# Optimization experiments

Measured on AMD Instinct MI355X. Metric: run time of the kernel, lower is better.

## Reference

```python
import math
import jax, jax.numpy as jnp
import numpy as np

B, S, D, H = 2, 2048, 1024, 16
DK = D // H


def setup_inputs() -> dict:
    key = jax.random.key(0)
    ks = jax.random.split(key, 12)
    scale = 1.0 / math.sqrt(D)
    inp = {
        "q": jax.random.normal(ks[0], (B, S, D), jnp.float32),
        "k": jax.random.normal(ks[1], (B, S, D), jnp.float32),
        "v": jax.random.normal(ks[2], (B, S, D), jnp.float32),
        # causal mask, broadcast over batch and heads (mask==0 -> -inf)
        "mask": jnp.tril(jnp.ones((S, S), jnp.int32))[None, None, :, :],
        "Wq": jax.random.normal(ks[3], (D, D), jnp.float32) * scale,
        "bq": jnp.zeros((D,), jnp.float32),
        "Wk": jax.random.normal(ks[4], (D, D), jnp.float32) * scale,
        "bk": jnp.zeros((D,), jnp.float32),
        "Wv": jax.random.normal(ks[5], (D, D), jnp.float32) * scale,
        "bv": jnp.zeros((D,), jnp.float32),
        "Wo": jax.random.normal(ks[6], (D, D), jnp.float32) * scale,
        "bo": jnp.zeros((D,), jnp.float32),
    }
    return inp


def reference(q, k, v, mask, Wq, bq, Wk, bk, Wv, bv, Wo, bo):
    def proj(x, W, b):
        # [B,S,D] -> [B,H,S,DK]
        return (x @ W + b).reshape(B, -1, H, DK).transpose(0, 2, 1, 3)

    Q = proj(q, Wq, bq)
    K = proj(k, Wk, bk)
    V = proj(v, Wv, bv)
    scores = jnp.einsum("bhqd,bhkd->bhqk", Q, K) / math.sqrt(DK)  # [B,H,S,S]
    scores = jnp.where(mask == 0, -jnp.inf, scores)
    attn = jax.nn.softmax(scores, axis=-1)  # dropout p=0.0 -> identity
    ctx = jnp.einsum("bhqk,bhkd->bhqd", attn, V)
    ctx = ctx.transpose(0, 2, 1, 3).reshape(B, -1, D)  # [B,S,D]
    return ctx @ Wo + bo
```

## Files before the change

### kernel.cpp

```cpp
#include <hip/hip_runtime.h>
#include <stdint.h>

#define BB 2
#define SS 2048
#define DD 1024
#define HH 16
#define DK 64

#define QSCALE 0.1803368801111204f
#define NEGS -1.0e30f

typedef short s16x8 __attribute__((ext_vector_type(8)));
typedef float f32x4 __attribute__((ext_vector_type(4)));
typedef unsigned short u16x4 __attribute__((ext_vector_type(4)));
typedef unsigned int u32x4 __attribute__((ext_vector_type(4)));

static __device__ __forceinline__ unsigned short f2bf(float f) {
  unsigned int u = __builtin_bit_cast(unsigned int, f);
  u = (u + 0x7fffu + ((u >> 16) & 1u)) >> 16;
  return (unsigned short)u;
}

static __device__ __forceinline__ float bf2f(unsigned short s) {
  unsigned int u = ((unsigned int)s) << 16;
  return __builtin_bit_cast(float, u);
}

static __device__ __forceinline__ unsigned int cvtpk(float lo, float hi) {
  unsigned int r;
  asm("v_cvt_pk_bf16_f32 %0, %1, %2" : "=v"(r) : "v"(lo), "v"(hi));
  return r;
}

static __device__ __forceinline__ f32x4 mfma16(s16x8 a, s16x8 b, f32x4 c) {
  return __builtin_amdgcn_mfma_f32_16x16x32_bf16(a, b, c, 0, 0, 0);
}

static __device__ __forceinline__ void gload_lds16(const void* g, void* l) {
  __builtin_amdgcn_global_load_lds(
      (const __attribute__((address_space(1))) unsigned int*)g,
      (__attribute__((address_space(3))) unsigned int*)l, 16, 0, 0);
}

__global__ __launch_bounds__(256) void cvt3_kernel(const float* __restrict__ q,
                                                   const float* __restrict__ k,
                                                   const float* __restrict__ v,
                                                   unsigned short* __restrict__ qb,
                                                   unsigned short* __restrict__ kb,
                                                   unsigned short* __restrict__ vb) {
  int sel = blockIdx.y;
  const float* in = (sel == 0) ? q : ((sel == 1) ? k : v);
  unsigned short* out = (sel == 0) ? qb : ((sel == 1) ? kb : vb);
  int i = blockIdx.x * 256 + threadIdx.x;
  f32x4 vv = ((const f32x4*)in)[i];
  u16x4 o;
  o.x = f2bf(vv.x); o.y = f2bf(vv.y); o.z = f2bf(vv.z); o.w = f2bf(vv.w);
  ((u16x4*)out)[i] = o;
}

__global__ __launch_bounds__(256) void transpose_w4_kernel(const float* __restrict__ Wq,
                                                           const float* __restrict__ Wk,
                                                           const float* __restrict__ Wv,
                                                           const float* __restrict__ Wo,
                                                           unsigned short* __restrict__ WTbase) {
  __shared__ float t[32][33];
  int z = blockIdx.z;
  const float* W = (z == 0) ? Wq : ((z == 1) ? Wk : ((z == 2) ? Wv : Wo));
  float scale = (z == 0) ? QSCALE : 1.0f;
  unsigned short* WT = WTbase + (size_t)z * DD * DD;
  int n0 = blockIdx.x * 32, k0 = blockIdx.y * 32;
  int tx = threadIdx.x, ty = threadIdx.y;
  for (int i = 0; i < 4; ++i)
    t[ty + 8 * i][tx] = W[(size_t)(k0 + ty + 8 * i) * DD + n0 + tx];
  __syncthreads();
  for (int i = 0; i < 4; ++i)
    WT[(size_t)(n0 + ty + 8 * i) * DD + k0 + tx] = f2bf(t[tx][ty + 8 * i] * scale);
}

__global__ __launch_bounds__(256) void transpose_v_kernel(const unsigned short* __restrict__ V,
                                                          unsigned short* __restrict__ VT) {
  __shared__ unsigned short t[32][33];
  int s0 = blockIdx.x * 32, d0 = blockIdx.y * 32, bh = blockIdx.z;
  int tx = threadIdx.x, ty = threadIdx.y;
  const unsigned short* Vb = V + (size_t)bh * SS * DK;
  unsigned short* Tb = VT + (size_t)bh * DK * SS;
  for (int i = 0; i < 4; ++i)
    t[ty + 8 * i][tx] = Vb[(size_t)(s0 + ty + 8 * i) * DK + d0 + tx];
  __syncthreads();
  for (int i = 0; i < 4; ++i)
    Tb[(size_t)(d0 + ty + 8 * i) * SS + s0 + tx] = t[tx][ty + 8 * i];
}

__global__ __launch_bounds__(256) void gemm_qkv_kernel(
    const unsigned short* __restrict__ qb, const unsigned short* __restrict__ kb,
    const unsigned short* __restrict__ vb, const unsigned short* __restrict__ WTbase,
    const float* __restrict__ bq, const float* __restrict__ bk,
    const float* __restrict__ bv, unsigned short* __restrict__ Qh,
    unsigned short* __restrict__ Kh, unsigned short* __restrict__ Vh) {
  const int K = DD;
  __shared__ __align__(16) unsigned short Alds[128 * 32];
  __shared__ __align__(16) unsigned short Blds[128 * 32];
  int tid = threadIdx.x;
  int lane = tid & 63, wave = tid >> 6;
  int g = lane >> 4, r16 = lane & 15;
  int seg = blockIdx.y >> 5;
  int m0 = (blockIdx.y & 31) * 128, n0 = blockIdx.x * 128;
  int wm = (wave >> 1) * 64, wn = (wave & 1) * 64;

  const unsigned short* A = (seg == 0) ? qb : ((seg == 1) ? kb : vb);
  const unsigned short* BT = WTbase + (size_t)seg * DD * DD;
  const float* bias = (seg == 0) ? bq : ((seg == 1) ? bk : bv);
  unsigned short* outh = (seg == 0) ? Qh : ((seg == 1) ? Kh : Vh);
  float bsc = (seg == 0) ? QSCALE : 1.0f;

  f32x4 acc[4][4] = {};

  int c0 = tid, c1 = tid + 256;
  int arow0 = c0 >> 2, arow1 = c1 >> 2;
  int as0 = (c0 & 3) ^ ((arow0 >> 1) & 3);
  int as1 = (c1 & 3) ^ ((arow1 >> 1) & 3);

  for (int k0 = 0; k0 < K; k0 += 32) {
    __syncthreads();
    gload_lds16((const char*)(A + (size_t)(m0 + arow0) * K + k0) + as0 * 16,
                (char*)Alds + wave * 1024);
    gload_lds16((const char*)(A + (size_t)(m0 + arow1) * K + k0) + as1 * 16,
                (char*)Alds + wave * 1024 + 4096);
    gload_lds16((const char*)(BT + (size_t)(n0 + arow0) * K + k0) + as0 * 16,
                (char*)Blds + wave * 1024);
    gload_lds16((const char*)(BT + (size_t)(n0 + arow1) * K + k0) + as1 * 16,
                (char*)Blds + wave * 1024 + 4096);
    __syncthreads();

    s16x8 af[4], bfr[4];
#pragma unroll
    for (int mt = 0; mt < 4; ++mt) {
      int row = wm + mt * 16 + r16;
      int ch = g ^ ((row >> 1) & 3);
      af[mt] = *(const s16x8*)((const char*)Alds + row * 64 + ch * 16);
    }
#pragma unroll
    for (int nt = 0; nt < 4; ++nt) {
      int row = wn + nt * 16 + r16;
      int ch = g ^ ((row >> 1) & 3);
      bfr[nt] = *(const s16x8*)((const char*)Blds + row * 64 + ch * 16);
    }
#pragma unroll
    for (int mt = 0; mt < 4; ++mt)
#pragma unroll
      for (int nt = 0; nt < 4; ++nt)
        acc[mt][nt] = mfma16(af[mt], bfr[nt], acc[mt][nt]);
  }

#pragma unroll
  for (int nt = 0; nt < 4; ++nt) {
    int col = n0 + wn + nt * 16 + r16;
    int h = col >> 6, dk = col & (DK - 1);
    float bvv = bias[col] * bsc;
#pragma unroll
    for (int mt = 0; mt < 4; ++mt) {
#pragma unroll
      for (int rr = 0; rr < 4; ++rr) {
        int rowg = m0 + wm + mt * 16 + g * 4 + rr;
        int bb = rowg >> 11, s = rowg & (SS - 1);
        float val = acc[mt][nt][rr] + bvv;
        outh[(((size_t)bb * HH + h) * SS + s) * DK + dk] = f2bf(val);
      }
    }
  }
}

__global__ __launch_bounds__(256) void gemm_out_kernel(const unsigned short* __restrict__ A,
                                                       const unsigned short* __restrict__ BT,
                                                       const float* __restrict__ bias,
                                                       float* __restrict__ out) {
  const int K = DD;
  __shared__ __align__(16) unsigned short Alds[128 * 32];
  __shared__ __align__(16) unsigned short Blds[64 * 32];
  int tid = threadIdx.x;
  int lane = tid & 63, wave = tid >> 6;
  int g = lane >> 4, r16 = lane & 15;
  int m0 = blockIdx.y * 128, n0 = blockIdx.x * 64;
  int wm = (wave >> 1) * 64, wn = (wave & 1) * 32;

  f32x4 acc[4][2] = {};

  int c0 = tid, c1 = tid + 256;
  int arow0 = c0 >> 2, arow1 = c1 >> 2;
  int as0 = (c0 & 3) ^ ((arow0 >> 1) & 3);
  int as1 = (c1 & 3) ^ ((arow1 >> 1) & 3);

  for (int k0 = 0; k0 < K; k0 += 32) {
    __syncthreads();
    gload_lds16((const char*)(A + (size_t)(m0 + arow0) * K + k0) + as0 * 16,
                (char*)Alds + wave * 1024);
    gload_lds16((const char*)(A + (size_t)(m0 + arow1) * K + k0) + as1 * 16,
                (char*)Alds + wave * 1024 + 4096);
    gload_lds16((const char*)(BT + (size_t)(n0 + arow0) * K + k0) + as0 * 16,
                (char*)Blds + wave * 1024);
    __syncthreads();

    s16x8 af[4], bfr[2];
#pragma unroll
    for (int mt = 0; mt < 4; ++mt) {
      int row = wm + mt * 16 + r16;
      int ch = g ^ ((row >> 1) & 3);
      af[mt] = *(const s16x8*)((const char*)Alds + row * 64 + ch * 16);
    }
#pragma unroll
    for (int nt = 0; nt < 2; ++nt) {
      int row = wn + nt * 16 + r16;
      int ch = g ^ ((row >> 1) & 3);
      bfr[nt] = *(const s16x8*)((const char*)Blds + row * 64 + ch * 16);
    }
#pragma unroll
    for (int mt = 0; mt < 4; ++mt)
#pragma unroll
      for (int nt = 0; nt < 2; ++nt)
        acc[mt][nt] = mfma16(af[mt], bfr[nt], acc[mt][nt]);
  }

#pragma unroll
  for (int nt = 0; nt < 2; ++nt) {
    int col = n0 + wn + nt * 16 + r16;
    float bvv = bias[col];
#pragma unroll
    for (int mt = 0; mt < 4; ++mt) {
#pragma unroll
      for (int rr = 0; rr < 4; ++rr) {
        int rowg = m0 + wm + mt * 16 + g * 4 + rr;
        out[(size_t)rowg * DD + col] = acc[mt][nt][rr] + bvv;
      }
    }
  }
}

__global__ __launch_bounds__(256) void attn_kernel(const unsigned short* __restrict__ Qh,
                                                   const unsigned short* __restrict__ Kh,
                                                   const unsigned short* __restrict__ VhT,
                                                   unsigned short* __restrict__ ctx,
                                                   unsigned short* __restrict__ Opart,
                                                   float2* __restrict__ mlpart) {
  __shared__ __align__(16) unsigned short Klds[2][64 * 64];
  __shared__ __align__(16) unsigned short Vlds[2][64 * 64];

  int tid = threadIdx.x;
  int lane = tid & 63, wave = tid >> 6;
  int g = lane >> 4, r16 = lane & 15;
  int bid = blockIdx.x;
  int x = bid >> 3;
  int pid = x & 15;
  int hf = (x >> 4) & 1;
  int bh = ((x >> 5) << 3) | (bid & 7);

  int tilesA = hf ? 0 : pid + 1;
  int NT = hf ? 16 : 17;
  int q0A = pid * 64, q0B = (31 - pid) * 64;
  int kvoffB = hf ? (16 - pid) : 0;

  const unsigned short* Qb = Qh + (size_t)bh * SS * DK;
  const char* Kb = (const char*)(Kh + (size_t)bh * SS * DK);
  const char* Vb = (const char*)(VhT + (size_t)bh * DK * SS);

  int a_ = r16 >> 2, b_ = r16 & 3;
  int rbase = 8 * a_ + b_;
  int sk = b_ + 4 * (a_ & 1);

  int c0 = tid, c1 = tid + 256;
  int row0 = c0 >> 3, row1 = c1 >> 3;
  int skst0 = ((row0 & 3) | (((row0 >> 3) & 1) << 2));
  int skst1 = ((row1 & 3) | (((row1 >> 3) & 1) << 2));
  int kc0 = (c0 & 7) ^ skst0, kc1 = (c1 & 7) ^ skst1;
  int vc0 = (c0 & 7) ^ (row0 & 7), vc1 = (c1 & 7) ^ (row1 & 7);

#define KV_OF(t) ((hf ? (kvoffB + (t)) : (((t) < tilesA) ? (t) : ((t) - tilesA))) * 64)
#define STAGE_KV(buf, kv0)                                                   \
  do {                                                                       \
    gload_lds16(Kb + ((size_t)((kv0) + row0) * 128) + kc0 * 16,              \
                (char*)Klds[buf] + wave * 1024);                             \
    gload_lds16(Kb + ((size_t)((kv0) + row1) * 128) + kc1 * 16,              \
                (char*)Klds[buf] + wave * 1024 + 4096);                      \
    gload_lds16(Vb + ((size_t)row0 * SS + (kv0)) * 2 + vc0 * 16,             \
                (char*)Vlds[buf] + wave * 1024);                             \
    gload_lds16(Vb + ((size_t)row1 * SS + (kv0)) * 2 + vc1 * 16,             \
                (char*)Vlds[buf] + wave * 1024 + 4096);                      \
  } while (0)

  int b = bh >> 4, h = bh & (HH - 1);

  int qw0 = (hf ? q0B : q0A) + wave * 16;
  s16x8 aq[2];
#pragma unroll
  for (int kc = 0; kc < 2; ++kc)
    aq[kc] = *(const s16x8*)(Qb + (size_t)(qw0 + r16) * DK + kc * 32 + g * 8);

  STAGE_KV(0, KV_OF(0));

  f32x4 accd[4] = {};
  float mrow = -INFINITY, lrow = 0.0f;

  for (int t = 0; t < NT; ++t) {
    if (hf == 0 && t == tilesA) {
      float inv = 1.0f / lrow;
      int srow = qw0 + r16;
#pragma unroll
      for (int dsub = 0; dsub < 4; ++dsub) {
        int d0 = dsub * 16 + 4 * g;
        u16x4 o;
#pragma unroll
        for (int rr = 0; rr < 4; ++rr) o[rr] = f2bf(accd[dsub][rr] * inv);
        *(u16x4*)&ctx[(((size_t)b * SS + srow) * HH + h) * DK + d0] = o;
      }
      qw0 = q0B + wave * 16;
#pragma unroll
      for (int kc = 0; kc < 2; ++kc)
        aq[kc] = *(const s16x8*)(Qb + (size_t)(qw0 + r16) * DK + kc * 32 + g * 8);
#pragma unroll
      for (int dsub = 0; dsub < 4; ++dsub) accd[dsub] = (f32x4){0.f, 0.f, 0.f, 0.f};
      mrow = -INFINITY;
      lrow = 0.0f;
    }

    int kv0 = KV_OF(t);

    __syncthreads();
    if (t + 1 < NT) STAGE_KV((t + 1) & 1, KV_OF(t + 1));

    const char* Kc = (const char*)Klds[t & 1];
    const char* Vc = (const char*)Vlds[t & 1];

    f32x4 sf[4] = {};
    __builtin_amdgcn_s_setprio(1);
#pragma unroll
    for (int kc = 0; kc < 2; ++kc) {
      s16x8 bk[4];
#pragma unroll
      for (int nt = 0; nt < 4; ++nt) {
        int row = rbase + 4 * (nt & 1) + 32 * (nt >> 1);
        int ch = (kc * 4 + g) ^ sk;
        bk[nt] = *(const s16x8*)(Kc + row * 128 + ch * 16);
      }
#pragma unroll
      for (int nt = 0; nt < 4; ++nt)
        sf[nt] = mfma16(bk[nt], aq[kc], sf[nt]);
    }
    __builtin_amdgcn_s_setprio(0);

    s16x8 av[2][4];
#pragma unroll
    for (int c = 0; c < 2; ++c)
#pragma unroll
      for (int dsub = 0; dsub < 4; ++dsub) {
        int row = dsub * 16 + r16;
        int ch = (c * 4 + g) ^ (row & 7);
        av[c][dsub] = *(const s16x8*)(Vc + row * 128 + ch * 16);
      }

    if (kv0 + 63 > qw0) {
      int thr = qw0 + r16 - kv0 - 8 * g;
#pragma unroll
      for (int nt = 0; nt < 4; ++nt) {
        int koff = 4 * (nt & 1) + 32 * (nt >> 1);
#pragma unroll
        for (int rr = 0; rr < 4; ++rr)
          if (koff + rr > thr) sf[nt][rr] = NEGS;
      }
    }

    float tmax = NEGS;
#pragma unroll
    for (int nt = 0; nt < 4; ++nt)
#pragma unroll
      for (int rr = 0; rr < 4; ++rr) tmax = fmaxf(tmax, sf[nt][rr]);
    tmax = fmaxf(tmax, __shfl_xor(tmax, 16));
    tmax = fmaxf(tmax, __shfl_xor(tmax, 32));

    if (!__all(tmax <= mrow)) {
      float mn = fmaxf(mrow, tmax);
      float fc = __builtin_amdgcn_exp2f(mrow - mn);
      lrow *= fc;
      mrow = mn;
#pragma unroll
      for (int dsub = 0; dsub < 4; ++dsub)
#pragma unroll
        for (int rr = 0; rr < 4; ++rr) accd[dsub][rr] *= fc;
    }

    float pf[4][4];
    float su = 0.0f;
#pragma unroll
    for (int nt = 0; nt < 4; ++nt)
#pragma unroll
      for (int rr = 0; rr < 4; ++rr) {
        float p = __builtin_amdgcn_exp2f(sf[nt][rr] - mrow);
        pf[nt][rr] = p;
        su += p;
      }
    su += __shfl_xor(su, 16);
    su += __shfl_xor(su, 32);
    lrow += su;

    unsigned int pk[2][4];
#pragma unroll
    for (int c = 0; c < 2; ++c) {
      pk[c][0] = cvtpk(pf[2 * c][0], pf[2 * c][1]);
      pk[c][1] = cvtpk(pf[2 * c][2], pf[2 * c][3]);
      pk[c][2] = cvtpk(pf[2 * c + 1][0], pf[2 * c + 1][1]);
      pk[c][3] = cvtpk(pf[2 * c + 1][2], pf[2 * c + 1][3]);
    }

    __builtin_amdgcn_s_setprio(1);
#pragma unroll
    for (int c = 0; c < 2; ++c) {
      s16x8 pb = __builtin_bit_cast(s16x8, *(u32x4*)pk[c]);
#pragma unroll
      for (int dsub = 0; dsub < 4; ++dsub)
        accd[dsub] = mfma16(av[c][dsub], pb, accd[dsub]);
    }
    __builtin_amdgcn_s_setprio(0);
  }

  size_t prow = ((size_t)bh * 16 + pid) * 64 + wave * 16 + r16;
  float inv = 1.0f / lrow;
  unsigned short* Op = Opart + ((size_t)hf * 32768 + prow) * 64;
#pragma unroll
  for (int dsub = 0; dsub < 4; ++dsub) {
    int d0 = dsub * 16 + 4 * g;
    u16x4 o;
#pragma unroll
    for (int rr = 0; rr < 4; ++rr) o[rr] = f2bf(accd[dsub][rr] * inv);
    *(u16x4*)&Op[d0] = o;
  }
  if (g == 0) mlpart[(size_t)hf * 32768 + prow] = make_float2(mrow, lrow);
#undef STAGE_KV
#undef KV_OF
}

__global__ __launch_bounds__(256) void combine_kernel(const unsigned short* __restrict__ Opart,
                                                      const float2* __restrict__ mlpart,
                                                      unsigned short* __restrict__ ctx) {
  int idx = blockIdx.x * 256 + threadIdx.x;
  int row = idx >> 4;
  int d0 = (idx & 15) * 4;
  float2 ml0 = mlpart[row];
  float2 ml1 = mlpart[32768 + row];
  float m = fmaxf(ml0.x, ml1.x);
  float w0 = __builtin_amdgcn_exp2f(ml0.x - m) * ml0.y;
  float w1 = __builtin_amdgcn_exp2f(ml1.x - m) * ml1.y;
  float inv = 1.0f / (w0 + w1);
  w0 *= inv;
  w1 *= inv;
  u16x4 a = *(const u16x4*)(Opart + (size_t)row * 64 + d0);
  u16x4 bb4 = *(const u16x4*)(Opart + ((size_t)32768 + row) * 64 + d0);
  u16x4 o;
#pragma unroll
  for (int j = 0; j < 4; ++j) o[j] = f2bf(bf2f(a[j]) * w0 + bf2f(bb4[j]) * w1);
  int p = row >> 6, rin = row & 63;
  int bh = p >> 4, pid = p & 15;
  int srow = (31 - pid) * 64 + rin;
  int b = bh >> 4, h = bh & (HH - 1);
  *(u16x4*)&ctx[(((size_t)b * SS + srow) * HH + h) * DK + d0] = o;
}

extern "C" void kernel_launch(void* const* d_in, const int* in_sizes, int n_in,
                              void* d_out, int out_size, void* d_ws, size_t ws_size,
                              hipStream_t stream) {
  const float* q = (const float*)d_in[0];
  const float* k = (const float*)d_in[1];
  const float* v = (const float*)d_in[2];
  const float* Wq = (const float*)d_in[4];
  const float* bq = (const float*)d_in[5];
  const float* Wk = (const float*)d_in[6];
  const float* bk = (const float*)d_in[7];
  const float* Wv = (const float*)d_in[8];
  const float* bv = (const float*)d_in[9];
  const float* Wo = (const float*)d_in[10];
  const float* bo = (const float*)d_in[11];

  char* ws = (char*)d_ws;
  const size_t MB = 1ull << 20;
  unsigned short* qb = (unsigned short*)(ws + 0 * MB);
  unsigned short* kb = (unsigned short*)(ws + 8 * MB);
  unsigned short* vb = (unsigned short*)(ws + 16 * MB);
  unsigned short* WTbase = (unsigned short*)(ws + 24 * MB);
  unsigned short* WoT = (unsigned short*)(ws + 30 * MB);
  unsigned short* Qh = (unsigned short*)(ws + 32 * MB);
  unsigned short* Kh = (unsigned short*)(ws + 40 * MB);
  unsigned short* Vh = (unsigned short*)(ws + 48 * MB);
  unsigned short* VhT = (unsigned short*)(ws + 16 * MB);
  unsigned short* ctx = (unsigned short*)(ws + 0 * MB);
  unsigned short* Opart = (unsigned short*)(ws + 8 * MB);
  float2* mlpart = (float2*)(ws + 24 * MB);

  const int n4 = BB * SS * DD / 4;

  cvt3_kernel<<<dim3(n4 / 256, 3), 256, 0, stream>>>(q, k, v, qb, kb, vb);

  dim3 tb(32, 8);
  transpose_w4_kernel<<<dim3(32, 32, 4), tb, 0, stream>>>(Wq, Wk, Wv, Wo, WTbase);

  gemm_qkv_kernel<<<dim3(8, 96), 256, 0, stream>>>(qb, kb, vb, WTbase,
                                                   bq, bk, bv, Qh, Kh, Vh);

  transpose_v_kernel<<<dim3(SS / 32, DK / 32, BB * HH), tb, 0, stream>>>(Vh, VhT);

  attn_kernel<<<1024, 256, 0, stream>>>(Qh, Kh, VhT, ctx, Opart, mlpart);

  combine_kernel<<<2048, 256, 0, stream>>>(Opart, mlpart, ctx);

  gemm_out_kernel<<<dim3(16, 32), 256, 0, stream>>>(ctx, WoT, bo, (float*)d_out);
}
```

Before: 132.9 us.

## Fuse V transpose into QKV GEMM epilogue and double attention query tile per wave

The QKV GEMM now writes V directly in transposed [bh, dk, s] layout with vectorized stores, which removes the separate transpose_v kernel launch and its extra pass over memory. The attention kernel processes 128 query rows per block (32 per wave, as two 16-row MFMA tiles) instead of 64. Each K/V tile staged in LDS is therefore reused for twice as many queries, and the grid halves to 512 blocks. The causal pairing and the combine indexing are adjusted to match. The cost is higher register pressure and fewer blocks to fill the GPU.

New measurement: 140.5 us. +5.7%, slower.

```diff
diff --git a/kernel.cpp b/kernel.cpp
--- a/kernel.cpp
+++ b/kernel.cpp
@@ -77,26 +77,12 @@
     WT[(size_t)(n0 + ty + 8 * i) * DD + k0 + tx] = f2bf(t[tx][ty + 8 * i] * scale);
 }
 
-__global__ __launch_bounds__(256) void transpose_v_kernel(const unsigned short* __restrict__ V,
-                                                          unsigned short* __restrict__ VT) {
-  __shared__ unsigned short t[32][33];
-  int s0 = blockIdx.x * 32, d0 = blockIdx.y * 32, bh = blockIdx.z;
-  int tx = threadIdx.x, ty = threadIdx.y;
-  const unsigned short* Vb = V + (size_t)bh * SS * DK;
-  unsigned short* Tb = VT + (size_t)bh * DK * SS;
-  for (int i = 0; i < 4; ++i)
-    t[ty + 8 * i][tx] = Vb[(size_t)(s0 + ty + 8 * i) * DK + d0 + tx];
-  __syncthreads();
-  for (int i = 0; i < 4; ++i)
-    Tb[(size_t)(d0 + ty + 8 * i) * SS + s0 + tx] = t[tx][ty + 8 * i];
-}
-
 __global__ __launch_bounds__(256) void gemm_qkv_kernel(
     const unsigned short* __restrict__ qb, const unsigned short* __restrict__ kb,
     const unsigned short* __restrict__ vb, const unsigned short* __restrict__ WTbase,
     const float* __restrict__ bq, const float* __restrict__ bk,
     const float* __restrict__ bv, unsigned short* __restrict__ Qh,
-    unsigned short* __restrict__ Kh, unsigned short* __restrict__ Vh) {
+    unsigned short* __restrict__ Kh, unsigned short* __restrict__ VhT) {
   const int K = DD;
   __shared__ __align__(16) unsigned short Alds[128 * 32];
   __shared__ __align__(16) unsigned short Blds[128 * 32];
@@ -110,7 +96,6 @@
   const unsigned short* A = (seg == 0) ? qb : ((seg == 1) ? kb : vb);
   const unsigned short* BT = WTbase + (size_t)seg * DD * DD;
   const float* bias = (seg == 0) ? bq : ((seg == 1) ? bk : bv);
-  unsigned short* outh = (seg == 0) ? Qh : ((seg == 1) ? Kh : Vh);
   float bsc = (seg == 0) ? QSCALE : 1.0f;
 
   f32x4 acc[4][4] = {};
@@ -152,6 +137,7 @@
         acc[mt][nt] = mfma16(af[mt], bfr[nt], acc[mt][nt]);
   }
 
+  unsigned short* outh = (seg == 0) ? Qh : Kh;
 #pragma unroll
   for (int nt = 0; nt < 4; ++nt) {
     int col = n0 + wn + nt * 16 + r16;
@@ -159,12 +145,19 @@
     float bvv = bias[col] * bsc;
 #pragma unroll
     for (int mt = 0; mt < 4; ++mt) {
-#pragma unroll
-      for (int rr = 0; rr < 4; ++rr) {
-        int rowg = m0 + wm + mt * 16 + g * 4 + rr;
-        int bb = rowg >> 11, s = rowg & (SS - 1);
-        float val = acc[mt][nt][rr] + bvv;
-        outh[(((size_t)bb * HH + h) * SS + s) * DK + dk] = f2bf(val);
+      int row0g = m0 + wm + mt * 16 + g * 4;
+      int bb = row0g >> 11, s0 = row0g & (SS - 1);
+      if (seg == 2) {
+        u16x4 o;
+#pragma unroll
+        for (int rr = 0; rr < 4; ++rr) o[rr] = f2bf(acc[mt][nt][rr] + bvv);
+        *(u16x4*)&VhT[((size_t)(bb * HH + h) * DK + dk) * SS + s0] = o;
+      } else {
+#pragma unroll
+        for (int rr = 0; rr < 4; ++rr) {
+          outh[(((size_t)bb * HH + h) * SS + s0 + rr) * DK + dk] =
+              f2bf(acc[mt][nt][rr] + bvv);
+        }
       }
     }
   }
@@ -249,14 +242,14 @@
   int g = lane >> 4, r16 = lane & 15;
   int bid = blockIdx.x;
   int x = bid >> 3;
-  int pid = x & 15;
-  int hf = (x >> 4) & 1;
-  int bh = ((x >> 5) << 3) | (bid & 7);
-
-  int tilesA = hf ? 0 : pid + 1;
-  int NT = hf ? 16 : 17;
-  int q0A = pid * 64, q0B = (31 - pid) * 64;
-  int kvoffB = hf ? (16 - pid) : 0;
+  int pid = x & 7;
+  int hf = (x >> 3) & 1;
+  int bh = ((x >> 4) << 3) | (bid & 7);
+
+  int tilesA = hf ? 0 : 2 * pid + 2;
+  const int NT = 17;
+  int q0A = pid * 128, q0B = (15 - pid) * 128;
+  int kvoffB = hf ? (15 - 2 * pid) : 0;
 
   const unsigned short* Qb = Qh + (size_t)bh * SS * DK;
   const char* Kb = (const char*)(Kh + (size_t)bh * SS * DK);
@@ -288,37 +281,48 @@
 
   int b = bh >> 4, h = bh & (HH - 1);
 
-  int qw0 = (hf ? q0B : q0A) + wave * 16;
-  s16x8 aq[2];
-#pragma unroll
-  for (int kc = 0; kc < 2; ++kc)
-    aq[kc] = *(const s16x8*)(Qb + (size_t)(qw0 + r16) * DK + kc * 32 + g * 8);
+  int qw0 = (hf ? q0B : q0A) + wave * 32;
+  s16x8 aq[2][2];
+#pragma unroll
+  for (int mt = 0; mt < 2; ++mt)
+#pragma unroll
+    for (int kc = 0; kc < 2; ++kc)
+      aq[mt][kc] = *(const s16x8*)(Qb + (size_t)(qw0 + mt * 16 + r16) * DK + kc * 32 + g * 8);
 
   STAGE_KV(0, KV_OF(0));
 
-  f32x4 accd[4] = {};
-  float mrow = -INFINITY, lrow = 0.0f;
+  f32x4 accd[2][4] = {};
+  float mrow[2] = {-INFINITY, -INFINITY};
+  float lrow[2] = {0.0f, 0.0f};
 
   for (int t = 0; t < NT; ++t) {
     if (hf == 0 && t == tilesA) {
-      float inv = 1.0f / lrow;
-      int srow = qw0 + r16;
-#pragma unroll
-      for (int dsub = 0; dsub < 4; ++dsub) {
-        int d0 = dsub * 16 + 4 * g;
-        u16x4 o;
-#pragma unroll
-        for (int rr = 0; rr < 4; ++rr) o[rr] = f2bf(accd[dsub][rr] * inv);
-        *(u16x4*)&ctx[(((size_t)b * SS + srow) * HH + h) * DK + d0] = o;
-      }
-      qw0 = q0B + wave * 16;
-#pragma unroll
-      for (int kc = 0; kc < 2; ++kc)
-        aq[kc] = *(const s16x8*)(Qb + (size_t)(qw0 + r16) * DK + kc * 32 + g * 8);
-#pragma unroll
-      for (int dsub = 0; dsub < 4; ++dsub) accd[dsub] = (f32x4){0.f, 0.f, 0.f, 0.f};
-      mrow = -INFINITY;
-      lrow = 0.0f;
+#pragma unroll
+      for (int mt = 0; mt < 2; ++mt) {
+        float inv = 1.0f / lrow[mt];
+        int srow = qw0 + mt * 16 + r16;
+#pragma unroll
+        for (int dsub = 0; dsub < 4; ++dsub) {
+          int d0 = dsub * 16 + 4 * g;
+          u16x4 o;
+#pragma unroll
+          for (int rr = 0; rr < 4; ++rr) o[rr] = f2bf(accd[mt][dsub][rr] * inv);
+          *(u16x4*)&ctx[(((size_t)b * SS + srow) * HH + h) * DK + d0] = o;
+        }
+      }
+      qw0 = q0B + wave * 32;
+#pragma unroll
+      for (int mt = 0; mt < 2; ++mt)
+#pragma unroll
+        for (int kc = 0; kc < 2; ++kc)
+          aq[mt][kc] = *(const s16x8*)(Qb + (size_t)(qw0 + mt * 16 + r16) * DK + kc * 32 + g * 8);
+#pragma unroll
+      for (int mt = 0; mt < 2; ++mt) {
+#pragma unroll
+        for (int dsub = 0; dsub < 4; ++dsub) accd[mt][dsub] = (f32x4){0.f, 0.f, 0.f, 0.f};
+        mrow[mt] = -INFINITY;
+        lrow[mt] = 0.0f;
+      }
     }
 
     int kv0 = KV_OF(t);
@@ -329,7 +333,7 @@
     const char* Kc = (const char*)Klds[t & 1];
     const char* Vc = (const char*)Vlds[t & 1];
 
-    f32x4 sf[4] = {};
+    f32x4 sf[2][4] = {};
     __builtin_amdgcn_s_setprio(1);
 #pragma unroll
     for (int kc = 0; kc < 2; ++kc) {
@@ -341,8 +345,10 @@
         bk[nt] = *(const s16x8*)(Kc + row * 128 + ch * 16);
       }
 #pragma unroll
-      for (int nt = 0; nt < 4; ++nt)
-        sf[nt] = mfma16(bk[nt], aq[kc], sf[nt]);
+      for (int nt = 0; nt < 4; ++nt) {
+        sf[0][nt] = mfma16(bk[nt], aq[0][kc], sf[0][nt]);
+        sf[1][nt] = mfma16(bk[nt], aq[1][kc], sf[1][nt]);
+      }
     }
     __builtin_amdgcn_s_setprio(0);
 
@@ -356,82 +362,93 @@
         av[c][dsub] = *(const s16x8*)(Vc + row * 128 + ch * 16);
       }
 
-    if (kv0 + 63 > qw0) {
-      int thr = qw0 + r16 - kv0 - 8 * g;
-#pragma unroll
-      for (int nt = 0; nt < 4; ++nt) {
-        int koff = 4 * (nt & 1) + 32 * (nt >> 1);
+    bool domask = (kv0 + 63 > qw0);
+    unsigned int pk[2][2][4];
+#pragma unroll
+    for (int mt = 0; mt < 2; ++mt) {
+      if (domask) {
+        int thr = qw0 + mt * 16 + r16 - kv0 - 8 * g;
+#pragma unroll
+        for (int nt = 0; nt < 4; ++nt) {
+          int koff = 4 * (nt & 1) + 32 * (nt >> 1);
+#pragma unroll
+          for (int rr = 0; rr < 4; ++rr)
+            if (koff + rr > thr) sf[mt][nt][rr] = NEGS;
+        }
+      }
+
+      float m0v = fmaxf(fmaxf(sf[mt][0][0], sf[mt][0][1]), fmaxf(sf[mt][0][2], sf[mt][0][3]));
+      float m1v = fmaxf(fmaxf(sf[mt][1][0], sf[mt][1][1]), fmaxf(sf[mt][1][2], sf[mt][1][3]));
+      float m2v = fmaxf(fmaxf(sf[mt][2][0], sf[mt][2][1]), fmaxf(sf[mt][2][2], sf[mt][2][3]));
+      float m3v = fmaxf(fmaxf(sf[mt][3][0], sf[mt][3][1]), fmaxf(sf[mt][3][2], sf[mt][3][3]));
+      float tmax = fmaxf(fmaxf(m0v, m1v), fmaxf(m2v, m3v));
+      tmax = fmaxf(tmax, __shfl_xor(tmax, 16));
+      tmax = fmaxf(tmax, __shfl_xor(tmax, 32));
+
+      if (!__all(tmax <= mrow[mt])) {
+        float mn = fmaxf(mrow[mt], tmax);
+        float fc = __builtin_amdgcn_exp2f(mrow[mt] - mn);
+        lrow[mt] *= fc;
+        mrow[mt] = mn;
+#pragma unroll
+        for (int dsub = 0; dsub < 4; ++dsub)
+#pragma unroll
+          for (int rr = 0; rr < 4; ++rr) accd[mt][dsub][rr] *= fc;
+      }
+
+      float pf[4][4];
+#pragma unroll
+      for (int nt = 0; nt < 4; ++nt)
 #pragma unroll
         for (int rr = 0; rr < 4; ++rr)
-          if (koff + rr > thr) sf[nt][rr] = NEGS;
-      }
-    }
-
-    float tmax = NEGS;
-#pragma unroll
-    for (int nt = 0; nt < 4; ++nt)
-#pragma unroll
-      for (int rr = 0; rr < 4; ++rr) tmax = fmaxf(tmax, sf[nt][rr]);
-    tmax = fmaxf(tmax, __shfl_xor(tmax, 16));
-    tmax = fmaxf(tmax, __shfl_xor(tmax, 32));
-
-    if (!__all(tmax <= mrow)) {
-      float mn = fmaxf(mrow, tmax);
-      float fc = __builtin_amdgcn_exp2f(mrow - mn);
-      lrow *= fc;
-      mrow = mn;
-#pragma unroll
-      for (int dsub = 0; dsub < 4; ++dsub)
-#pragma unroll
-        for (int rr = 0; rr < 4; ++rr) accd[dsub][rr] *= fc;
-    }
-
-    float pf[4][4];
-    float su = 0.0f;
-#pragma unroll
-    for (int nt = 0; nt < 4; ++nt)
-#pragma unroll
-      for (int rr = 0; rr < 4; ++rr) {
-        float p = __builtin_amdgcn_exp2f(sf[nt][rr] - mrow);
-        pf[nt][rr] = p;
-        su += p;
-      }
-    su += __shfl_xor(su, 16);
-    su += __shfl_xor(su, 32);
-    lrow += su;
-
-    unsigned int pk[2][4];
+          pf[nt][rr] = __builtin_amdgcn_exp2f(sf[mt][nt][rr] - mrow[mt]);
+      float s0v = (pf[0][0] + pf[0][1]) + (pf[0][2] + pf[0][3]);
+      float s1v = (pf[1][0] + pf[1][1]) + (pf[1][2] + pf[1][3]);
+      float s2v = (pf[2][0] + pf[2][1]) + (pf[2][2] + pf[2][3]);
+      float s3v = (pf[3][0] + pf[3][1]) + (pf[3][2] + pf[3][3]);
+      float su = (s0v + s1v) + (s2v + s3v);
+      su += __shfl_xor(su, 16);
+      su += __shfl_xor(su, 32);
+      lrow[mt] += su;
+
+#pragma unroll
+      for (int c = 0; c < 2; ++c) {
+        pk[mt][c][0] = cvtpk(pf[2 * c][0], pf[2 * c][1]);
+        pk[mt][c][1] = cvtpk(pf[2 * c][2], pf[2 * c][3]);
+        pk[mt][c][2] = cvtpk(pf[2 * c + 1][0], pf[2 * c + 1][1]);
+        pk[mt][c][3] = cvtpk(pf[2 * c + 1][2], pf[2 * c + 1][3]);
+      }
+    }
+
+    __builtin_amdgcn_s_setprio(1);
 #pragma unroll
     for (int c = 0; c < 2; ++c) {
-      pk[c][0] = cvtpk(pf[2 * c][0], pf[2 * c][1]);
-      pk[c][1] = cvtpk(pf[2 * c][2], pf[2 * c][3]);
-      pk[c][2] = cvtpk(pf[2 * c + 1][0], pf[2 * c + 1][1]);
-      pk[c][3] = cvtpk(pf[2 * c + 1][2], pf[2 * c + 1][3]);
-    }
-
-    __builtin_amdgcn_s_setprio(1);
-#pragma unroll
-    for (int c = 0; c < 2; ++c) {
-      s16x8 pb = __builtin_bit_cast(s16x8, *(u32x4*)pk[c]);
-#pragma unroll
-      for (int dsub = 0; dsub < 4; ++dsub)
-        accd[dsub] = mfma16(av[c][dsub], pb, accd[dsub]);
+      s16x8 pb0 = __builtin_bit_cast(s16x8, *(u32x4*)pk[0][c]);
+      s16x8 pb1 = __builtin_bit_cast(s16x8, *(u32x4*)pk[1][c]);
+#pragma unroll
+      for (int dsub = 0; dsub < 4; ++dsub) {
+        accd[0][dsub] = mfma16(av[c][dsub], pb0, accd[0][dsub]);
+        accd[1][dsub] = mfma16(av[c][dsub], pb1, accd[1][dsub]);
+      }
     }
     __builtin_amdgcn_s_setprio(0);
   }
 
-  size_t prow = ((size_t)bh * 16 + pid) * 64 + wave * 16 + r16;
-  float inv = 1.0f / lrow;
-  unsigned short* Op = Opart + ((size_t)hf * 32768 + prow) * 64;
-#pragma unroll
-  for (int dsub = 0; dsub < 4; ++dsub) {
-    int d0 = dsub * 16 + 4 * g;
-    u16x4 o;
-#pragma unroll
-    for (int rr = 0; rr < 4; ++rr) o[rr] = f2bf(accd[dsub][rr] * inv);
-    *(u16x4*)&Op[d0] = o;
+#pragma unroll
+  for (int mt = 0; mt < 2; ++mt) {
+    size_t prow = ((size_t)bh * 8 + pid) * 128 + wave * 32 + mt * 16 + r16;
+    float inv = 1.0f / lrow[mt];
+    unsigned short* Op = Opart + ((size_t)hf * 32768 + prow) * 64;
+#pragma unroll
+    for (int dsub = 0; dsub < 4; ++dsub) {
+      int d0 = dsub * 16 + 4 * g;
+      u16x4 o;
+#pragma unroll
+      for (int rr = 0; rr < 4; ++rr) o[rr] = f2bf(accd[mt][dsub][rr] * inv);
+      *(u16x4*)&Op[d0] = o;
+    }
+    if (g == 0) mlpart[(size_t)hf * 32768 + prow] = make_float2(mrow[mt], lrow[mt]);
   }
-  if (g == 0) mlpart[(size_t)hf * 32768 + prow] = make_float2(mrow, lrow);
 #undef STAGE_KV
 #undef KV_OF
 }
@@ -455,9 +472,9 @@
   u16x4 o;
 #pragma unroll
   for (int j = 0; j < 4; ++j) o[j] = f2bf(bf2f(a[j]) * w0 + bf2f(bb4[j]) * w1);
-  int p = row >> 6, rin = row & 63;
-  int bh = p >> 4, pid = p & 15;
-  int srow = (31 - pid) * 64 + rin;
+  int p = row >> 7, rin = row & 127;
+  int bh = p >> 3, pid = p & 7;
+  int srow = (15 - pid) * 128 + rin;
   int b = bh >> 4, h = bh & (HH - 1);
   *(u16x4*)&ctx[(((size_t)b * SS + srow) * HH + h) * DK + d0] = o;
 }
@@ -486,8 +503,7 @@
   unsigned short* WoT = (unsigned short*)(ws + 30 * MB);
   unsigned short* Qh = (unsigned short*)(ws + 32 * MB);
   unsigned short* Kh = (unsigned short*)(ws + 40 * MB);
-  unsigned short* Vh = (unsigned short*)(ws + 48 * MB);
-  unsigned short* VhT = (unsigned short*)(ws + 16 * MB);
+  unsigned short* VhT = (unsigned short*)(ws + 48 * MB);
   unsigned short* ctx = (unsigned short*)(ws + 0 * MB);
   unsigned short* Opart = (unsigned short*)(ws + 8 * MB);
   float2* mlpart = (float2*)(ws + 24 * MB);
@@ -500,11 +516,9 @@
   transpose_w4_kernel<<<dim3(32, 32, 4), tb, 0, stream>>>(Wq, Wk, Wv, Wo, WTbase);
 
   gemm_qkv_kernel<<<dim3(8, 96), 256, 0, stream>>>(qb, kb, vb, WTbase,
-                                                   bq, bk, bv, Qh, Kh, Vh);
-
-  transpose_v_kernel<<<dim3(SS / 32, DK / 32, BB * HH), tb, 0, stream>>>(Vh, VhT);
-
-  attn_kernel<<<1024, 256, 0, stream>>>(Qh, Kh, VhT, ctx, Opart, mlpart);
+                                                   bq, bk, bv, Qh, Kh, VhT);
+
+  attn_kernel<<<512, 256, 0, stream>>>(Qh, Kh, VhT, ctx, Opart, mlpart);
 
   combine_kernel<<<2048, 256, 0, stream>>>(Opart, mlpart, ctx);
 
```
